# Performance work log

Hardware: AMD Instinct MI355X
Metric: run time of the kernel (lower is better)

Reference implementation:

```python
import jax, jax.numpy as jnp
import numpy as np
from jax import lax

EPS = 1e-06


def setup_inputs() -> dict:
    key = jax.random.key(0)
    B, MICS, T, F = 16, 4, 2048, 257
    x = jax.random.uniform(key, (B, MICS, T, F), dtype=jnp.float32)
    s = jnp.array([0.025], dtype=jnp.float32)
    alpha = jnp.array([0.98], dtype=jnp.float32)
    delta = jnp.array([2.0], dtype=jnp.float32)
    r = jnp.array([0.5], dtype=jnp.float32)
    return {"x": x, "s": s, "alpha": alpha, "delta": delta, "r": r}


def reference(x, s, alpha, delta, r):
    # x: [batch, mics, chans, frames]; EMA recurrence runs over dim 2 (split dim -2 in source)
    B, MICS, T, F = x.shape
    xr = x.reshape(B * MICS, T, F)
    xt = jnp.moveaxis(xr, 1, 0)  # [T, BM, F] -- scan axis first

    s0 = s[0]

    def step(carry, frame):
        m = (1.0 - s0) * carry + s0 * frame
        return m, m

    m0 = xt[0]  # first frame: M_0 = x_0 (last_state=None branch)
    _, ms = lax.scan(step, m0, xt[1:])
    M = jnp.concatenate([m0[None], ms], axis=0)  # [T, BM, F]
    M = jnp.moveaxis(M, 0, 1)  # [BM, T, F]

    # pcen nonlinearity: (x / (M+eps)^alpha + delta)^r - delta^r
    out = jnp.power(xr / jnp.power(M + EPS, alpha) + delta, r) - jnp.power(delta, r)
    return out.reshape(B, MICS, T, F)
```

## Files before the change

kernel.cpp:

```cpp
#include <hip/hip_runtime.h>
#include <hip/hip_bf16.h>


#define EPS 1e-6f

constexpr int BM = 64;
constexpr int T  = 2048;
constexpr int F  = 257;
constexpr int L  = 128;
constexpr int C  = T / L;
constexpr int H  = 256;
constexpr int NWORK = BM * C * F;
constexpr int BATCH = 16;

__device__ __forceinline__ float fast_exp2(float x) { return __builtin_amdgcn_exp2f(x); }
__device__ __forceinline__ float fast_log2(float x) { return __builtin_amdgcn_logf(x); }

__device__ __forceinline__ float pcen_nl(float xv, float m, float alpha,
                                         float delta, float r, float dr) {
  float inner = fmaf(xv, fast_exp2(-alpha * fast_log2(m + EPS)), delta);
  return fast_exp2(r * fast_log2(inner)) - dr;
}

__global__ __launch_bounds__(256) void pcen_fused(
    const float* __restrict__ x, const float* __restrict__ s_p,
    const float* __restrict__ alpha_p, const float* __restrict__ delta_p,
    const float* __restrict__ r_p, float* __restrict__ out) {
  int idx = blockIdx.x * 256 + threadIdx.x;

  const float s     = s_p[0];
  const float a     = 1.0f - s;
  const float alpha = alpha_p[0];
  const float delta = delta_p[0];
  const float r     = r_p[0];
  const float dr    = fast_exp2(r * fast_log2(delta));

  int bm  = idx / (C * F);
  int rem = idx - bm * (C * F);
  int c   = rem / F;
  int f   = rem - c * F;

  const size_t col = (size_t)bm * T * F + f;
  const float* xcol = x + col;
  float*       ocol = out + col;

  const int tstart = c * L;
  int t0 = tstart - H;
  if (t0 < 0) t0 = 0;

  float m;
  int t;
  if (t0 == 0) {
    m = xcol[0];
    t = 0;
  } else {
    m = 0.0f;
    t = t0;
  }

  {
    const float* p = xcol + (size_t)t * F;
    int nwarm = tstart - t;
    for (int b = 0; b < nwarm; b += BATCH) {
      float xv[BATCH];
      #pragma unroll
      for (int k = 0; k < BATCH; ++k) xv[k] = p[k * F];
      #pragma unroll
      for (int k = 0; k < BATCH; ++k) m = fmaf(a, m, s * xv[k]);
      p += BATCH * F;
    }
  }

  {
    const float* p  = xcol + (size_t)tstart * F;
    float*       op = ocol + (size_t)tstart * F;
    for (int b = 0; b < L / BATCH; ++b) {
      float xv[BATCH];
      #pragma unroll
      for (int k = 0; k < BATCH; ++k) xv[k] = p[k * F];
      #pragma unroll
      for (int k = 0; k < BATCH; ++k) {
        m = fmaf(a, m, s * xv[k]);
        float o = pcen_nl(xv[k], m, alpha, delta, r, dr);
        __builtin_nontemporal_store(o, &op[k * F]);
      }
      p  += BATCH * F;
      op += BATCH * F;
    }
  }
}

extern "C" void kernel_launch(void* const* d_in, const int* in_sizes, int n_in,
                              void* d_out, int out_size, void* d_ws, size_t ws_size,
                              hipStream_t stream) {
  const float* x     = (const float*)d_in[0];
  const float* s     = (const float*)d_in[1];
  const float* alpha = (const float*)d_in[2];
  const float* delta = (const float*)d_in[3];
  const float* r     = (const float*)d_in[4];
  float* out = (float*)d_out;

  const int blocks = NWORK / 256;
  pcen_fused<<<blocks, 256, 0, stream>>>(x, s, alpha, delta, r, out);
}
```

Measured before the change: 300.0 us.

## Stream time tiles via global-to-LDS DMA with double buffering per wave

Replaces the one-thread-per-column kernel with one 64-lane wave per (signal, chunk). Each wave loads 16-frame tiles straight into LDS with global_load_lds and double-buffers them using explicit waitcnt. The EMA and PCEN are computed from LDS and written back in place, and the tile is then stored as 16-byte nontemporal vectors. This is meant to keep more memory traffic in flight and to use wider, fully coalesced accesses. The cost is a very small grid of single-wave blocks, so there is little latency hiding across waves, plus hand-encoded wait counts that are fragile.

```diff
diff --git a/kernel.cpp b/kernel.cpp
--- a/kernel.cpp
+++ b/kernel.cpp
@@ -1,17 +1,17 @@
 #include <hip/hip_runtime.h>
-#include <hip/hip_bf16.h>
 
 
 #define EPS 1e-6f
 
-constexpr int BM = 64;
-constexpr int T  = 2048;
-constexpr int F  = 257;
-constexpr int L  = 128;
-constexpr int C  = T / L;
-constexpr int H  = 256;
-constexpr int NWORK = BM * C * F;
-constexpr int BATCH = 16;
+constexpr int T   = 2048;
+constexpr int F   = 257;
+constexpr int L   = 128;
+constexpr int NCH = T / L;
+constexpr int TFR = 16;
+constexpr int TILE_BYTES = TFR * F * 4;
+constexpr int OUT_TILES  = L / TFR;
+
+typedef float f32x4 __attribute__((ext_vector_type(4)));
 
 __device__ __forceinline__ float fast_exp2(float x) { return __builtin_amdgcn_exp2f(x); }
 __device__ __forceinline__ float fast_log2(float x) { return __builtin_amdgcn_logf(x); }
@@ -22,11 +22,25 @@
   return fast_exp2(r * fast_log2(inner)) - dr;
 }
 
-__global__ __launch_bounds__(256) void pcen_fused(
+typedef const __attribute__((address_space(1))) unsigned int* gas1;
+typedef __attribute__((address_space(3))) unsigned int* las3;
+
+__device__ __forceinline__ void dma16(const void* g, void* l) {
+  __builtin_amdgcn_global_load_lds((gas1)g, (las3)l, 16, 0, 0);
+}
+
+constexpr int wenc(int vm) {
+  return (vm & 15) | (7 << 4) | (15 << 8) | ((vm >> 4) << 14);
+}
+
+__global__ __launch_bounds__(64, 1) void pcen_dma(
     const float* __restrict__ x, const float* __restrict__ s_p,
     const float* __restrict__ alpha_p, const float* __restrict__ delta_p,
     const float* __restrict__ r_p, float* __restrict__ out) {
-  int idx = blockIdx.x * 256 + threadIdx.x;
+  __shared__ f32x4 slots[2][TFR * F / 4];
+  const int lane = threadIdx.x;
+  const int bm   = blockIdx.x >> 4;
+  const int c    = blockIdx.x & (NCH - 1);
 
   const float s     = s_p[0];
   const float a     = 1.0f - s;
@@ -35,57 +49,86 @@
   const float r     = r_p[0];
   const float dr    = fast_exp2(r * fast_log2(delta));
 
-  int bm  = idx / (C * F);
-  int rem = idx - bm * (C * F);
-  int c   = rem / F;
-  int f   = rem - c * F;
+  const int  warmT  = (c == 0) ? 0 : (c == 1 ? 8 : 16);
+  const int  NT     = warmT + OUT_TILES;
+  const bool exact0 = (c <= 1);
+  const int  startFrame = (c <= 1) ? 0 : (c * L - 256);
 
-  const size_t col = (size_t)bm * T * F + f;
-  const float* xcol = x + col;
-  float*       ocol = out + col;
+  const char* gx   = (const char*)x  + ((size_t)bm * T + (size_t)startFrame) * (F * 4);
+  char*       gout = (char*)out      + ((size_t)bm * T + (size_t)c * L) * (F * 4);
 
-  const int tstart = c * L;
-  int t0 = tstart - H;
-  if (t0 < 0) t0 = 0;
+  auto issue = [&](int ti) {
+    const char* g = gx + (size_t)ti * TILE_BYTES;
+    char* lb = (char*)&slots[ti & 1][0];
+    #pragma unroll
+    for (int k = 0; k < 16; ++k)
+      dma16(g + k * 1024 + lane * 16, lb + k * 1024);
+    if (lane < 4)
+      dma16(g + 16384 + lane * 16, lb + 16384);
+  };
 
-  float m;
-  int t;
-  if (t0 == 0) {
-    m = xcol[0];
-    t = 0;
-  } else {
-    m = 0.0f;
-    t = t0;
-  }
+  issue(0);
+  float m0 = 0.f, m1 = 0.f, m2 = 0.f, m3 = 0.f, m4 = 0.f;
 
-  {
-    const float* p = xcol + (size_t)t * F;
-    int nwarm = tstart - t;
-    for (int b = 0; b < nwarm; b += BATCH) {
-      float xv[BATCH];
+  for (int ti = 0; ti < NT; ++ti) {
+    if (ti + 1 < NT) issue(ti + 1);
+    __builtin_amdgcn_sched_barrier(0);
+    const bool nxt = (ti + 1 < NT);
+    const bool pst = (ti >= 1) && (ti - 1 >= warmT);
+    if (nxt && pst)      __builtin_amdgcn_s_waitcnt(wenc(34));
+    else if (nxt || pst) __builtin_amdgcn_s_waitcnt(wenc(17));
+    else                 __builtin_amdgcn_s_waitcnt(wenc(0));
+    __builtin_amdgcn_sched_barrier(0);
+
+    float* sp = (float*)&slots[ti & 1][0];
+
+    if (ti < warmT) {
       #pragma unroll
-      for (int k = 0; k < BATCH; ++k) xv[k] = p[k * F];
+      for (int f = 0; f < TFR; ++f) {
+        float x0 = sp[f * F + lane];
+        float x1 = sp[f * F + 64 + lane];
+        float x2 = sp[f * F + 128 + lane];
+        float x3 = sp[f * F + 192 + lane];
+        float x4 = sp[f * F + 256];
+        if (exact0 && ti == 0 && f == 0) {
+          m0 = x0; m1 = x1; m2 = x2; m3 = x3; m4 = x4;
+        }
+        m0 = fmaf(a, m0, s * x0); m1 = fmaf(a, m1, s * x1);
+        m2 = fmaf(a, m2, s * x2); m3 = fmaf(a, m3, s * x3);
+        m4 = fmaf(a, m4, s * x4);
+      }
+    } else {
       #pragma unroll
-      for (int k = 0; k < BATCH; ++k) m = fmaf(a, m, s * xv[k]);
-      p += BATCH * F;
-    }
-  }
-
-  {
-    const float* p  = xcol + (size_t)tstart * F;
-    float*       op = ocol + (size_t)tstart * F;
-    for (int b = 0; b < L / BATCH; ++b) {
-      float xv[BATCH];
+      for (int f = 0; f < TFR; ++f) {
+        float x0 = sp[f * F + lane];
+        float x1 = sp[f * F + 64 + lane];
+        float x2 = sp[f * F + 128 + lane];
+        float x3 = sp[f * F + 192 + lane];
+        float x4 = sp[f * F + 256];
+        if (exact0 && ti == 0 && f == 0) {
+          m0 = x0; m1 = x1; m2 = x2; m3 = x3; m4 = x4;
+        }
+        m0 = fmaf(a, m0, s * x0); m1 = fmaf(a, m1, s * x1);
+        m2 = fmaf(a, m2, s * x2); m3 = fmaf(a, m3, s * x3);
+        m4 = fmaf(a, m4, s * x4);
+        sp[f * F + lane]       = pcen_nl(x0, m0, alpha, delta, r, dr);
+        sp[f * F + 64 + lane]  = pcen_nl(x1, m1, alpha, delta, r, dr);
+        sp[f * F + 128 + lane] = pcen_nl(x2, m2, alpha, delta, r, dr);
+        sp[f * F + 192 + lane] = pcen_nl(x3, m3, alpha, delta, r, dr);
+        if (lane == 0)
+          sp[f * F + 256] = pcen_nl(x4, m4, alpha, delta, r, dr);
+      }
+      char* go = gout + (size_t)(ti - warmT) * TILE_BYTES;
+      char* lb = (char*)sp;
       #pragma unroll
-      for (int k = 0; k < BATCH; ++k) xv[k] = p[k * F];
-      #pragma unroll
-      for (int k = 0; k < BATCH; ++k) {
-        m = fmaf(a, m, s * xv[k]);
-        float o = pcen_nl(xv[k], m, alpha, delta, r, dr);
-        __builtin_nontemporal_store(o, &op[k * F]);
+      for (int k = 0; k < 16; ++k) {
+        f32x4 v = *(const f32x4*)(lb + k * 1024 + lane * 16);
+        __builtin_nontemporal_store(v, (f32x4*)(go + k * 1024 + lane * 16));
       }
-      p  += BATCH * F;
-      op += BATCH * F;
+      if (lane < 4) {
+        f32x4 v = *(const f32x4*)(lb + 16384 + lane * 16);
+        __builtin_nontemporal_store(v, (f32x4*)(go + 16384 + lane * 16));
+      }
     }
   }
 }
@@ -100,6 +143,5 @@
   const float* r     = (const float*)d_in[4];
   float* out = (float*)d_out;
 
-  const int blocks = NWORK / 256;
-  pcen_fused<<<blocks, 256, 0, stream>>>(x, s, alpha, delta, r, out);
+  pcen_dma<<<64 * NCH, 64, 0, stream>>>(x, s, alpha, delta, r, out);
 }
```

Measured after the change: 286.5 us. 1.05x faster.
